# Kernel tuning notes

Hardware: AMD Instinct MI355X
Metric: run time of the kernel (lower is better)

## Reference

```python
import jax, jax.numpy as jnp
import numpy as np
import math

EPS = 1e-12  # matches F.normalize eps


def _l2_normalize(x):
    # F.normalize(x, p=2, dim=1): x / max(||x||, eps)
    n = jnp.sqrt(jnp.sum(x * x, axis=-1, keepdims=True))
    return x / jnp.maximum(n, EPS)


def setup_inputs() -> dict:
    key = jax.random.key(0)
    k1, k2 = jax.random.split(key)
    B, C, D = 4096, 10000, 1024
    features = jax.random.normal(k1, (B, D), dtype=jnp.float32)
    prototypes = jax.random.normal(k2, (C, D), dtype=jnp.float32)
    distance_scale = jnp.ones((1,), dtype=jnp.float32)
    temperature = jnp.ones((1,), dtype=jnp.float32)
    return {"features": features, "prototypes": prototypes,
            "distance_scale": distance_scale, "temperature": temperature}


def reference(features, prototypes, distance_scale, temperature):
    f = _l2_normalize(features)          # [B, D]
    p = _l2_normalize(prototypes)        # [C, D]
    # ||f - p||^2 = 2 - 2 f.p for unit vectors; clamp tiny negatives from fp error
    sq = jnp.maximum(2.0 - 2.0 * jnp.einsum('bd,cd->bc', f, p), EPS)
    dist = jnp.sqrt(sq) / math.sqrt(2.0)                      # [B, C]
    iso = jnp.abs(distance_scale) * dist                      # [B, C]
    logits = -(iso + jnp.mean(iso, axis=1, keepdims=True))
    return logits / temperature
```

## Files before the change

kernel.cpp:

```cpp
#include <hip/hip_runtime.h>
#include <hip/hip_bf16.h>

typedef __attribute__((ext_vector_type(8))) short short8;
typedef __attribute__((ext_vector_type(4))) float f32x4;

#define GLOBAL_AS __attribute__((address_space(1)))
#define LDS_AS    __attribute__((address_space(3)))

__device__ __forceinline__ void async_ld16(const void* g, void* l) {
    __builtin_amdgcn_global_load_lds((const GLOBAL_AS void*)g, (LDS_AS void*)l, 16, 0, 0);
}

__device__ __forceinline__ unsigned short f2bf(float x) {
    union { __hip_bfloat16 h; unsigned short u; } cv;
    cv.h = __float2bfloat16(x);
    return cv.u;
}

__global__ __launch_bounds__(256) void norm_rows_kernel(
    const float* __restrict__ in, unsigned short* __restrict__ outb, int rows_in)
{
    const int row = blockIdx.x;
    const int tid = threadIdx.x;
    float4 v = make_float4(0.f, 0.f, 0.f, 0.f);
    if (row < rows_in)
        v = reinterpret_cast<const float4*>(in + (size_t)row * 1024)[tid];
    float s = v.x * v.x + v.y * v.y + v.z * v.z + v.w * v.w;
    #pragma unroll
    for (int off = 32; off > 0; off >>= 1) s += __shfl_down(s, off);
    __shared__ float sr[4];
    if ((tid & 63) == 0) sr[tid >> 6] = s;
    __syncthreads();
    const float tot = sr[0] + sr[1] + sr[2] + sr[3];
    const float inv = 1.f / fmaxf(sqrtf(tot), 1e-12f);
    ushort4 o;
    o.x = f2bf(v.x * inv);
    o.y = f2bf(v.y * inv);
    o.z = f2bf(v.z * inv);
    o.w = f2bf(v.w * inv);
    reinterpret_cast<ushort4*>(outb + (size_t)row * 1024)[tid] = o;
}

__global__ __launch_bounds__(256) void gemm_iso_kernel(
    const unsigned short* __restrict__ A,
    const unsigned short* __restrict__ B,
    float* __restrict__ out,
    const float* __restrict__ ds_ptr,
    int M, int C, int K)
{
    __shared__ __align__(16) char As[128 * 64 * 2];
    __shared__ __align__(16) char Bs[128 * 64 * 2];

    const int tid  = threadIdx.x;
    const int lane = tid & 63;
    const int wid  = tid >> 6;
    const int brow = blockIdx.y * 128;
    const int bcol = blockIdx.x * 128;

    const int lrow8 = lane >> 3;
    const int slotg = (lane & 7) ^ lrow8;
    const size_t kb = (size_t)K * 2;

    const char* gA[4]; const char* gB[4]; char* lA[4]; char* lB[4];
    #pragma unroll
    for (int i = 0; i < 4; ++i) {
        const int seg = wid * 4 + i;
        const int r = seg * 8 + lrow8;
        gA[i] = (const char*)A + (size_t)(brow + r) * kb + slotg * 16;
        gB[i] = (const char*)B + (size_t)(bcol + r) * kb + slotg * 16;
        lA[i] = As + seg * 1024;
        lB[i] = Bs + seg * 1024;
    }

    const int wr = (wid >> 1) * 64;
    const int wc = (wid & 1) * 64;
    const int lr = lane & 15;
    const int kq = lane >> 4;
    const int sx = lane & 7;

    f32x4 zero = {0.f, 0.f, 0.f, 0.f};
    f32x4 acc[4][4];
    #pragma unroll
    for (int m = 0; m < 4; ++m)
        #pragma unroll
        for (int n = 0; n < 4; ++n)
            acc[m][n] = zero;

    int aoff[4], boff[4];
    #pragma unroll
    for (int m = 0; m < 4; ++m) {
        aoff[m] = (wr + m * 16 + lr) * 128;
        boff[m] = (wc + m * 16 + lr) * 128;
    }
    const int so0 = ((0 + kq) ^ sx) * 16;
    const int so1 = ((4 + kq) ^ sx) * 16;

    const int ksteps = K >> 6;
    for (int kt = 0; kt < ksteps; ++kt) {
        const size_t koff = (size_t)kt * 128;
        #pragma unroll
        for (int i = 0; i < 4; ++i) {
            async_ld16(gA[i] + koff, lA[i]);
            async_ld16(gB[i] + koff, lB[i]);
        }
        __syncthreads();
        #pragma unroll
        for (int kk = 0; kk < 2; ++kk) {
            const int so = kk ? so1 : so0;
            short8 a[4], b[4];
            #pragma unroll
            for (int m = 0; m < 4; ++m)
                a[m] = *reinterpret_cast<const short8*>(As + aoff[m] + so);
            #pragma unroll
            for (int n = 0; n < 4; ++n)
                b[n] = *reinterpret_cast<const short8*>(Bs + boff[n] + so);
            #pragma unroll
            for (int m = 0; m < 4; ++m)
                #pragma unroll
                for (int n = 0; n < 4; ++n)
                    acc[m][n] = __builtin_amdgcn_mfma_f32_16x16x32_bf16(
                        a[m], b[n], acc[m][n], 0, 0, 0);
        }
        __syncthreads();
    }

    const float dsv = fabsf(ds_ptr[0]);
    #pragma unroll
    for (int m = 0; m < 4; ++m) {
        const int row0 = brow + wr + m * 16 + kq * 4;
        #pragma unroll
        for (int n = 0; n < 4; ++n) {
            const int col = bcol + wc + n * 16 + lr;
            if (col < C) {
                float* op = out + (size_t)row0 * C + col;
                #pragma unroll
                for (int j = 0; j < 4; ++j) {
                    const float sq = fmaxf(2.f - 2.f * acc[m][n][j], 1e-12f);
                    op[(size_t)j * C] = dsv * (sqrtf(sq) * 0.70710678118654752f);
                }
            }
        }
    }
}

__global__ __launch_bounds__(256) void finalize_kernel(
    float* __restrict__ out, const float* __restrict__ tptr, int C)
{
    __shared__ float buf[10240];
    __shared__ float sred[4];
    const int row = blockIdx.x;
    const int tid = threadIdx.x;
    float* rp = out + (size_t)row * C;
    const int nv = C >> 2;
    float s = 0.f;
    for (int i = tid; i < nv; i += 256) {
        float4 v = reinterpret_cast<const float4*>(rp)[i];
        reinterpret_cast<float4*>(buf)[i] = v;
        s += (v.x + v.y) + (v.z + v.w);
    }
    for (int i = (nv << 2) + tid; i < C; i += 256) { float v = rp[i]; buf[i] = v; s += v; }
    #pragma unroll
    for (int off = 32; off > 0; off >>= 1) s += __shfl_down(s, off);
    if ((tid & 63) == 0) sred[tid >> 6] = s;
    __syncthreads();
    const float mean = (sred[0] + sred[1] + sred[2] + sred[3]) / (float)C;
    const float invT = 1.f / tptr[0];
    for (int i = tid; i < nv; i += 256) {
        float4 v = reinterpret_cast<const float4*>(buf)[i];
        float4 o;
        o.x = -(v.x + mean) * invT;
        o.y = -(v.y + mean) * invT;
        o.z = -(v.z + mean) * invT;
        o.w = -(v.w + mean) * invT;
        reinterpret_cast<float4*>(rp)[i] = o;
    }
    for (int i = (nv << 2) + tid; i < C; i += 256) rp[i] = -(buf[i] + mean) * invT;
}

extern "C" void kernel_launch(void* const* d_in, const int* in_sizes, int n_in,
                              void* d_out, int out_size, void* d_ws, size_t ws_size,
                              hipStream_t stream)
{
    const float* feat = (const float*)d_in[0];
    const float* prot = (const float*)d_in[1];
    const float* dsc  = (const float*)d_in[2];
    const float* temp = (const float*)d_in[3];
    float* out = (float*)d_out;

    const int D = 1024;
    const int M = in_sizes[0] / D;
    const int C = in_sizes[1] / D;
    const int NT = (C + 127) / 128;
    const int Npad = NT * 128;

    unsigned short* fbf = (unsigned short*)d_ws;
    unsigned short* pbf = fbf + (size_t)M * D;

    norm_rows_kernel<<<M, 256, 0, stream>>>(feat, fbf, M);
    norm_rows_kernel<<<Npad, 256, 0, stream>>>(prot, pbf, C);
    gemm_iso_kernel<<<dim3(NT, M / 128), 256, 0, stream>>>(fbf, pbf, out, dsc, M, C, D);
    finalize_kernel<<<M, 256, 0, stream>>>(out, temp, C);
}
```

Before: 371.5 us.

## Use 256x256 double-buffered GEMM tiles and fuse row-mean reduction into epilogue

Restructures the bf16 MFMA GEMM to 256x256 output tiles with 512 threads and a double-buffered 128KB LDS pipeline. It adds an XCD-aware block swizzle and raises wave priority around the MFMA loop. The epilogue now accumulates per-row sums of the iso distances and adds them to a zeroed workspace with atomics. This lets the finalize kernel become a simple elementwise pass with no per-row reduction or LDS staging. The cost is nondeterministic float atomic summation, heavier register and LDS use that limits occupancy, and one extra tiny zeroing launch.

```diff
diff --git a/kernel.cpp b/kernel.cpp
--- a/kernel.cpp
+++ b/kernel.cpp
@@ -41,140 +41,179 @@
     reinterpret_cast<ushort4*>(outb + (size_t)row * 1024)[tid] = o;
 }
 
-__global__ __launch_bounds__(256) void gemm_iso_kernel(
+__global__ __launch_bounds__(256) void zero_f32_kernel(float* __restrict__ p, int n)
+{
+    const int i = blockIdx.x * 256 + threadIdx.x;
+    if (i < n) p[i] = 0.f;
+}
+
+__global__ __launch_bounds__(512, 2) void gemm_iso_kernel(
     const unsigned short* __restrict__ A,
     const unsigned short* __restrict__ B,
     float* __restrict__ out,
+    float* __restrict__ rowsum,
     const float* __restrict__ ds_ptr,
     int M, int C, int K)
 {
-    __shared__ __align__(16) char As[128 * 64 * 2];
-    __shared__ __align__(16) char Bs[128 * 64 * 2];
+    __shared__ __align__(16) char lds[131072];
+
+    const float dsv_raw = ds_ptr[0];
 
     const int tid  = threadIdx.x;
     const int lane = tid & 63;
     const int wid  = tid >> 6;
-    const int brow = blockIdx.y * 128;
-    const int bcol = blockIdx.x * 128;
+
+    const int nwg  = gridDim.x * gridDim.y;
+    const int orig = blockIdx.y * gridDim.x + blockIdx.x;
+    const int cpx  = nwg >> 3;
+    const int swz  = (orig & 7) * cpx + (orig >> 3);
+    const int bx   = swz % gridDim.x;
+    const int by   = swz / gridDim.x;
+    const int brow = by * 256;
+    const int bcol = bx * 256;
 
     const int lrow8 = lane >> 3;
     const int slotg = (lane & 7) ^ lrow8;
     const size_t kb = (size_t)K * 2;
 
-    const char* gA[4]; const char* gB[4]; char* lA[4]; char* lB[4];
+    const char* pA[4]; const char* pB[4]; int lA[4], lB[4];
     #pragma unroll
     for (int i = 0; i < 4; ++i) {
         const int seg = wid * 4 + i;
-        const int r = seg * 8 + lrow8;
-        gA[i] = (const char*)A + (size_t)(brow + r) * kb + slotg * 16;
-        gB[i] = (const char*)B + (size_t)(bcol + r) * kb + slotg * 16;
-        lA[i] = As + seg * 1024;
-        lB[i] = Bs + seg * 1024;
+        const int r   = seg * 8 + lrow8;
+        pA[i] = (const char*)A + (size_t)(brow + r) * kb + slotg * 16;
+        pB[i] = (const char*)B + (size_t)(bcol + r) * kb + slotg * 16;
+        lA[i] = seg * 1024;
+        lB[i] = 32768 + seg * 1024;
     }
 
-    const int wr = (wid >> 1) * 64;
-    const int wc = (wid & 1) * 64;
+    auto STAGE = [&](int buf) {
+        char* base = lds + (buf << 16);
+        #pragma unroll
+        for (int i = 0; i < 4; ++i) async_ld16(pA[i], base + lA[i]);
+        #pragma unroll
+        for (int i = 0; i < 4; ++i) async_ld16(pB[i], base + lB[i]);
+        #pragma unroll
+        for (int i = 0; i < 4; ++i) { pA[i] += 128; pB[i] += 128; }
+    };
+
+    const int wr = (wid >> 2) * 128;
+    const int wc = (wid & 3) * 64;
     const int lr = lane & 15;
     const int kq = lane >> 4;
-    const int sx = lane & 7;
-
-    f32x4 zero = {0.f, 0.f, 0.f, 0.f};
-    f32x4 acc[4][4];
-    #pragma unroll
-    for (int m = 0; m < 4; ++m)
+    const int sx = lr & 7;
+
+    f32x4 acc[8][4];
+    #pragma unroll
+    for (int m = 0; m < 8; ++m)
         #pragma unroll
         for (int n = 0; n < 4; ++n)
-            acc[m][n] = zero;
-
-    int aoff[4], boff[4];
-    #pragma unroll
-    for (int m = 0; m < 4; ++m) {
-        aoff[m] = (wr + m * 16 + lr) * 128;
-        boff[m] = (wc + m * 16 + lr) * 128;
-    }
+            acc[m][n] = (f32x4){0.f, 0.f, 0.f, 0.f};
+
+    int aoff[8], boff[4];
+    #pragma unroll
+    for (int m = 0; m < 8; ++m) aoff[m] = (wr + m * 16 + lr) * 128;
+    #pragma unroll
+    for (int n = 0; n < 4; ++n) boff[n] = 32768 + (wc + n * 16 + lr) * 128;
     const int so0 = ((0 + kq) ^ sx) * 16;
     const int so1 = ((4 + kq) ^ sx) * 16;
 
-    const int ksteps = K >> 6;
-    for (int kt = 0; kt < ksteps; ++kt) {
-        const size_t koff = (size_t)kt * 128;
-        #pragma unroll
-        for (int i = 0; i < 4; ++i) {
-            async_ld16(gA[i] + koff, lA[i]);
-            async_ld16(gB[i] + koff, lB[i]);
-        }
-        __syncthreads();
+    auto COMPUTE = [&](int buf) {
+        const char* base = lds + (buf << 16);
         #pragma unroll
         for (int kk = 0; kk < 2; ++kk) {
             const int so = kk ? so1 : so0;
-            short8 a[4], b[4];
-            #pragma unroll
-            for (int m = 0; m < 4; ++m)
-                a[m] = *reinterpret_cast<const short8*>(As + aoff[m] + so);
+            short8 a[8], b[4];
+            #pragma unroll
+            for (int m = 0; m < 8; ++m)
+                a[m] = *reinterpret_cast<const short8*>(base + aoff[m] + so);
             #pragma unroll
             for (int n = 0; n < 4; ++n)
-                b[n] = *reinterpret_cast<const short8*>(Bs + boff[n] + so);
-            #pragma unroll
-            for (int m = 0; m < 4; ++m)
+                b[n] = *reinterpret_cast<const short8*>(base + boff[n] + so);
+            __builtin_amdgcn_s_setprio(1);
+            #pragma unroll
+            for (int m = 0; m < 8; ++m)
                 #pragma unroll
                 for (int n = 0; n < 4; ++n)
                     acc[m][n] = __builtin_amdgcn_mfma_f32_16x16x32_bf16(
                         a[m], b[n], acc[m][n], 0, 0, 0);
-        }
-        __syncthreads();
+            __builtin_amdgcn_s_setprio(0);
+        }
+    };
+
+    const int nt = K >> 6;
+    STAGE(0);
+    STAGE(1);
+    asm volatile("s_waitcnt vmcnt(8)" ::: "memory");
+    __builtin_amdgcn_s_barrier();
+    __builtin_amdgcn_sched_barrier(0);
+
+    for (int t = 0; t < nt; ++t) {
+        COMPUTE(t & 1);
+        if (t + 1 < nt) {
+            __builtin_amdgcn_s_barrier();
+            __builtin_amdgcn_sched_barrier(0);
+            if (t + 2 < nt) {
+                STAGE(t & 1);
+                asm volatile("s_waitcnt vmcnt(8)" ::: "memory");
+            } else {
+                asm volatile("s_waitcnt vmcnt(0)" ::: "memory");
+            }
+            __builtin_amdgcn_s_barrier();
+            __builtin_amdgcn_sched_barrier(0);
+        }
     }
 
-    const float dsv = fabsf(ds_ptr[0]);
-    #pragma unroll
-    for (int m = 0; m < 4; ++m) {
+    const float dsv = fabsf(dsv_raw);
+    #pragma unroll
+    for (int m = 0; m < 8; ++m) {
+        float rs0 = 0.f, rs1 = 0.f, rs2 = 0.f, rs3 = 0.f;
         const int row0 = brow + wr + m * 16 + kq * 4;
         #pragma unroll
         for (int n = 0; n < 4; ++n) {
             const int col = bcol + wc + n * 16 + lr;
-            if (col < C) {
-                float* op = out + (size_t)row0 * C + col;
-                #pragma unroll
-                for (int j = 0; j < 4; ++j) {
-                    const float sq = fmaxf(2.f - 2.f * acc[m][n][j], 1e-12f);
-                    op[(size_t)j * C] = dsv * (sqrtf(sq) * 0.70710678118654752f);
-                }
+            const bool ok = col < C;
+            float* op = out + (size_t)row0 * C + col;
+            #pragma unroll
+            for (int j = 0; j < 4; ++j) {
+                const float sq  = fmaxf(2.f - 2.f * acc[m][n][j], 1e-12f);
+                const float iso = dsv * (sqrtf(sq) * 0.70710678118654752f);
+                if (ok) op[(size_t)j * C] = iso;
+                const float c = ok ? iso : 0.f;
+                if (j == 0) rs0 += c; else if (j == 1) rs1 += c;
+                else if (j == 2) rs2 += c; else rs3 += c;
             }
         }
+        float r4[4] = {rs0, rs1, rs2, rs3};
+        #pragma unroll
+        for (int j = 0; j < 4; ++j) {
+            float r = r4[j];
+            r += __shfl_xor(r, 1);
+            r += __shfl_xor(r, 2);
+            r += __shfl_xor(r, 4);
+            r += __shfl_xor(r, 8);
+            if (lr == 0) atomicAdd(&rowsum[row0 + j], r);
+        }
     }
 }
 
 __global__ __launch_bounds__(256) void finalize_kernel(
-    float* __restrict__ out, const float* __restrict__ tptr, int C)
-{
-    __shared__ float buf[10240];
-    __shared__ float sred[4];
-    const int row = blockIdx.x;
-    const int tid = threadIdx.x;
+    float* __restrict__ out, const float* __restrict__ rowsum,
+    const float* __restrict__ tptr, int C)
+{
+    const int row = blockIdx.y;
+    const int i4  = blockIdx.x * 256 + threadIdx.x;
+    const int n4  = C >> 2;
+    if (i4 >= n4) return;
+    const float mean = rowsum[row] / (float)C;
+    const float invT = 1.f / tptr[0];
     float* rp = out + (size_t)row * C;
-    const int nv = C >> 2;
-    float s = 0.f;
-    for (int i = tid; i < nv; i += 256) {
-        float4 v = reinterpret_cast<const float4*>(rp)[i];
-        reinterpret_cast<float4*>(buf)[i] = v;
-        s += (v.x + v.y) + (v.z + v.w);
-    }
-    for (int i = (nv << 2) + tid; i < C; i += 256) { float v = rp[i]; buf[i] = v; s += v; }
-    #pragma unroll
-    for (int off = 32; off > 0; off >>= 1) s += __shfl_down(s, off);
-    if ((tid & 63) == 0) sred[tid >> 6] = s;
-    __syncthreads();
-    const float mean = (sred[0] + sred[1] + sred[2] + sred[3]) / (float)C;
-    const float invT = 1.f / tptr[0];
-    for (int i = tid; i < nv; i += 256) {
-        float4 v = reinterpret_cast<const float4*>(buf)[i];
-        float4 o;
-        o.x = -(v.x + mean) * invT;
-        o.y = -(v.y + mean) * invT;
-        o.z = -(v.z + mean) * invT;
-        o.w = -(v.w + mean) * invT;
-        reinterpret_cast<float4*>(rp)[i] = o;
-    }
-    for (int i = (nv << 2) + tid; i < C; i += 256) rp[i] = -(buf[i] + mean) * invT;
+    float4 v = reinterpret_cast<const float4*>(rp)[i4];
+    v.x = -(v.x + mean) * invT;
+    v.y = -(v.y + mean) * invT;
+    v.z = -(v.z + mean) * invT;
+    v.w = -(v.w + mean) * invT;
+    reinterpret_cast<float4*>(rp)[i4] = v;
 }
 
 extern "C" void kernel_launch(void* const* d_in, const int* in_sizes, int n_in,
@@ -190,14 +229,16 @@
     const int D = 1024;
     const int M = in_sizes[0] / D;
     const int C = in_sizes[1] / D;
-    const int NT = (C + 127) / 128;
-    const int Npad = NT * 128;
-
-    unsigned short* fbf = (unsigned short*)d_ws;
+    const int NT = (C + 255) / 256;
+    const int Npad = NT * 256;
+
+    float* rowsum = (float*)d_ws;
+    unsigned short* fbf = (unsigned short*)(rowsum + M);
     unsigned short* pbf = fbf + (size_t)M * D;
 
     norm_rows_kernel<<<M, 256, 0, stream>>>(feat, fbf, M);
     norm_rows_kernel<<<Npad, 256, 0, stream>>>(prot, pbf, C);
-    gemm_iso_kernel<<<dim3(NT, M / 128), 256, 0, stream>>>(fbf, pbf, out, dsc, M, C, D);
-    finalize_kernel<<<M, 256, 0, stream>>>(out, temp, C);
-}
+    zero_f32_kernel<<<(M + 255) / 256, 256, 0, stream>>>(rowsum, M);
+    gemm_iso_kernel<<<dim3(NT, M / 256), 512, 0, stream>>>(fbf, pbf, out, rowsum, dsc, M, C, D);
+    finalize_kernel<<<dim3((C / 4 + 255) / 256, M), 256, 0, stream>>>(out, rowsum, temp, C);
+}
```

Result: slower. 386.8 us (+4.1%).
